# Performance work log

Measured on AMD Instinct MI355X. Metric: run time of the kernel, lower is better.

## Reference

```python
import jax, jax.numpy as jnp
import numpy as np

B, GX, GY = 4, 480, 360
C_IN, C_OUT = 64, 32
N = 480000

def setup_inputs() -> dict:
    key = jax.random.key(0)
    k1, k2, k3, k4, k5 = jax.random.split(key, 5)
    pt_fea = jax.random.normal(k1, (N, C_IN), dtype=jnp.float32)
    pt_ind = jax.random.randint(k2, (N, 2), 0, 360, dtype=jnp.int32)
    batch_idx = jax.random.randint(k3, (N,), 0, B, dtype=jnp.int32)
    W_comp = jax.random.normal(k4, (C_IN, C_OUT), dtype=jnp.float32) * 0.1
    b_comp = jax.random.normal(k5, (C_OUT,), dtype=jnp.float32) * 0.1
    return {"pt_fea": pt_fea, "pt_ind": pt_ind, "batch_idx": batch_idx,
            "W_comp": W_comp, "b_comp": b_comp}

def reference(pt_fea, pt_ind, batch_idx, W_comp, b_comp):
    # Linearized voxel key: (batch, x, y) -> flat segment id.
    # torch.unique + scatter_max over unique voxels followed by fancy-index
    # scatter into a zero grid is equivalent to a dense segment_max with
    # empty voxels forced to zero.
    seg = (batch_idx.astype(jnp.int32) * (GX * GY)
           + pt_ind[:, 0] * GY + pt_ind[:, 1])  # [N]
    num_seg = B * GX * GY
    pooled = jax.ops.segment_max(pt_fea, seg, num_segments=num_seg)  # [BV, C_IN]
    cnt = jax.ops.segment_sum(jnp.ones((pt_fea.shape[0],), jnp.float32), seg,
                              num_segments=num_seg)  # [BV]
    occupied = (cnt > 0)[:, None]
    pooled = jnp.where(occupied, pooled, 0.0)  # neutralize -inf of empty voxels
    # fea_compression: Linear + ReLU, applied to occupied voxels only
    comp = jax.nn.relu(pooled @ W_comp + b_comp)  # [BV, C_OUT]
    comp = jnp.where(occupied, comp, 0.0)
    out = comp.reshape(B, GX, GY, C_OUT)
    return jnp.transpose(out, (0, 3, 1, 2))  # [B, C_OUT, GX, GY]
```

## Files before the change

### kernel.cpp

```cpp
#include <hip/hip_runtime.h>

#define GXGY  172800
#define NSEG  691200
#define CIN   64
#define COUT  32
#define VPB   64
#define PSTR  65
#define NTILE 675


__global__ __launch_bounds__(256) void count_kernel(
    const int* __restrict__ ind,
    const int* __restrict__ bidx,
    int*       __restrict__ cnt,
    int N)
{
    int i = blockIdx.x * 256 + threadIdx.x;
    if (i >= N) return;
    int2 xy = ((const int2*)ind)[i];
    int seg = bidx[i] * GXGY + xy.x * 360 + xy.y;
    atomicAdd(&cnt[seg], 1);
}

__global__ __launch_bounds__(256) void scan_tile_kernel(
    int* __restrict__ cnt, int* __restrict__ tsum)
{
    int t = threadIdx.x;
    int base = blockIdx.x * 256 + t;
    int4 c = ((const int4*)cnt)[base];
    int s = c.x + c.y + c.z + c.w;

    int lane = t & 63, wid = t >> 6;
    int v = s;
    #pragma unroll
    for (int d = 1; d < 64; d <<= 1) {
        int u = __shfl_up(v, d);
        if (lane >= d) v += u;
    }
    __shared__ int wsum[4];
    if (lane == 63) wsum[wid] = v;
    __syncthreads();
    int wbase = 0;
    #pragma unroll
    for (int w = 0; w < 3; ++w) if (w < wid) wbase += wsum[w];

    int excl = wbase + v - s;
    int4 o; o.x = excl; o.y = o.x + c.x; o.z = o.y + c.y; o.w = o.z + c.z;
    ((int4*)cnt)[base] = o;
    if (t == 255) tsum[blockIdx.x] = excl + s;
}

__global__ __launch_bounds__(256) void scan_totals_kernel(int* __restrict__ tsum)
{
    __shared__ int buf[1024];
    int t = threadIdx.x;
    for (int j = t; j < 1024; j += 256) buf[j] = (j < NTILE) ? tsum[j] : 0;
    __syncthreads();
    for (int d = 1; d < 1024; d <<= 1) {
        int vals[4];
        #pragma unroll
        for (int k = 0; k < 4; ++k) { int j = t + k * 256; vals[k] = (j >= d) ? buf[j - d] : 0; }
        __syncthreads();
        #pragma unroll
        for (int k = 0; k < 4; ++k) { int j = t + k * 256; buf[j] += vals[k]; }
        __syncthreads();
    }
    for (int j = t; j < NTILE; j += 256) tsum[j] = (j == 0) ? 0 : buf[j - 1];
}

__global__ __launch_bounds__(256) void fill_kernel(
    const int* __restrict__ ind,
    const int* __restrict__ bidx,
    int*       __restrict__ cnt,
    const int* __restrict__ tsum,
    int*       __restrict__ csr,
    int N)
{
    int i = blockIdx.x * 256 + threadIdx.x;
    if (i >= N) return;
    int2 xy = ((const int2*)ind)[i];
    int seg = bidx[i] * GXGY + xy.x * 360 + xy.y;
    int pos = atomicAdd(&cnt[seg], 1) + tsum[seg >> 10];
    csr[pos] = i;
}

__global__ __launch_bounds__(256) void pool_compress_kernel(
    const float* __restrict__ fea,
    const int*   __restrict__ cnt,
    const int*   __restrict__ tsum,
    const int*   __restrict__ csr,
    const float* __restrict__ W,
    const float* __restrict__ bias,
    float*       __restrict__ out)
{
    __shared__ float sP[VPB * PSTR];
    __shared__ int   sLen[VPB];
    __shared__ int   sIdx[4][64];

    int tid  = threadIdx.x;
    int wid  = tid >> 6;
    int lane = tid & 63;
    int sub  = lane >> 4;
    int sl   = lane & 15;

    int vbase = blockIdx.x * VPB;
    int v0    = vbase + wid * 16;

    int o = 0;
    if (lane < 17) {
        int vv = v0 - 1 + lane;
        o = (vv < 0) ? 0 : (cnt[vv] + tsum[vv >> 10]);
    }
    int onext = __shfl(o, (lane + 1) & 63);
    if (lane < 16) sLen[wid * 16 + lane] = onext - o;

    int ws0 = __shfl(o, 0);
    int wsE = __shfl(o, 16);
    int cw  = wsE - ws0;
    if (lane < min(cw, 64)) sIdx[wid][lane] = csr[ws0 + lane];

    int stt[4], len[4];
    #pragma unroll
    for (int q = 0; q < 4; ++q) {
        int a = __shfl(o, q * 4 + sub);
        int b = __shfl(o, q * 4 + sub + 1);
        stt[q] = a; len[q] = b - a;
    }
    int maxlen = max(max(len[0], len[1]), max(len[2], len[3]));

    float4 m[4];
    #pragma unroll
    for (int q = 0; q < 4; ++q) if (len[q] > 0) {
        int off = stt[q] - ws0;
        int id  = (off < 64) ? sIdx[wid][off] : csr[stt[q]];
        m[q] = ((const float4*)(fea + (size_t)id * CIN))[sl];
    }
    for (int r = 1; r < maxlen; ++r) {
        #pragma unroll
        for (int q = 0; q < 4; ++q) if (r < len[q]) {
            int off = stt[q] - ws0 + r;
            int id  = (off < 64) ? sIdx[wid][off] : csr[stt[q] + r];
            float4 t = ((const float4*)(fea + (size_t)id * CIN))[sl];
            m[q].x = fmaxf(m[q].x, t.x);
            m[q].y = fmaxf(m[q].y, t.y);
            m[q].z = fmaxf(m[q].z, t.z);
            m[q].w = fmaxf(m[q].w, t.w);
        }
    }
    #pragma unroll
    for (int q = 0; q < 4; ++q) if (len[q] > 0) {
        int lv = wid * 16 + q * 4 + sub;
        float* dst = &sP[lv * PSTR + sl * 4];
        dst[0] = m[q].x; dst[1] = m[q].y; dst[2] = m[q].z; dst[3] = m[q].w;
    }
    __syncthreads();

    int lv = lane;
    int g  = __builtin_amdgcn_readfirstlane(wid);
    int b  = vbase / GXGY;
    int rem = vbase - b * GXGY + lv;

    const float* Wg = W + g * 8;
    const float* bg = bias + g * 8;

    float res[8];
    if (sLen[lv] > 0) {
        float acc[8];
        #pragma unroll
        for (int c = 0; c < 8; ++c) acc[c] = bg[c];
        #pragma unroll 16
        for (int k = 0; k < CIN; ++k) {
            float p = sP[lv * PSTR + k];
            #pragma unroll
            for (int c = 0; c < 8; ++c)
                acc[c] = fmaf(p, Wg[k * COUT + c], acc[c]);
        }
        #pragma unroll
        for (int c = 0; c < 8; ++c) res[c] = fmaxf(acc[c], 0.0f);
    } else {
        #pragma unroll
        for (int c = 0; c < 8; ++c) res[c] = 0.0f;
    }

    float* op = out + (size_t)b * COUT * GXGY + (size_t)g * 8 * GXGY + rem;
    #pragma unroll
    for (int c = 0; c < 8; ++c) op[c * GXGY] = res[c];
}

extern "C" void kernel_launch(void* const* d_in, const int* in_sizes, int n_in,
                              void* d_out, int out_size, void* d_ws, size_t ws_size,
                              hipStream_t stream)
{
    const float* fea  = (const float*)d_in[0];
    const int*   ind  = (const int*)d_in[1];
    const int*   bidx = (const int*)d_in[2];
    const float* W    = (const float*)d_in[3];
    const float* bias = (const float*)d_in[4];
    float*       out  = (float*)d_out;

    int N = in_sizes[0] / CIN;

    int* cnt  = (int*)d_ws;
    int* tsum = cnt + NSEG;
    int* csr  = tsum + 1024;

    hipMemsetAsync(cnt, 0, (size_t)NSEG * sizeof(int), stream);
    count_kernel<<<(N + 255) / 256, 256, 0, stream>>>(ind, bidx, cnt, N);
    scan_tile_kernel<<<NTILE, 256, 0, stream>>>(cnt, tsum);
    scan_totals_kernel<<<1, 256, 0, stream>>>(tsum);
    fill_kernel<<<(N + 255) / 256, 256, 0, stream>>>(ind, bidx, cnt, tsum, csr, N);
    pool_compress_kernel<<<NSEG / VPB, 256, 0, stream>>>(fea, cnt, tsum, csr, W, bias, out);
}
```

Before: 294.8 us.

## Fold tile offsets into counts and batch gather loads for more memory-level parallelism

Adds a kernel that adds per-tile scan bases into the count array, so the fill and pool kernels no longer read tsum on every access. The pool kernel's gather loop for the common case (all of a wave's point indices cached in LDS) now issues 16 independent feature loads per iteration using clamped, branch-free indexing, which raises the number of memory requests in flight. Clamped lanes reload rows they already hold, adding redundant loads, and the change costs one extra kernel launch.

```diff
diff --git a/kernel.cpp b/kernel.cpp
--- a/kernel.cpp
+++ b/kernel.cpp
@@ -68,11 +68,20 @@
     for (int j = t; j < NTILE; j += 256) tsum[j] = (j == 0) ? 0 : buf[j - 1];
 }
 
+__global__ __launch_bounds__(256) void add_base_kernel(
+    int* __restrict__ cnt, const int* __restrict__ tsum)
+{
+    int t = tsum[blockIdx.x];
+    int4* p = (int4*)cnt + blockIdx.x * 256 + threadIdx.x;
+    int4 v = *p;
+    v.x += t; v.y += t; v.z += t; v.w += t;
+    *p = v;
+}
+
 __global__ __launch_bounds__(256) void fill_kernel(
     const int* __restrict__ ind,
     const int* __restrict__ bidx,
     int*       __restrict__ cnt,
-    const int* __restrict__ tsum,
     int*       __restrict__ csr,
     int N)
 {
@@ -80,14 +89,13 @@
     if (i >= N) return;
     int2 xy = ((const int2*)ind)[i];
     int seg = bidx[i] * GXGY + xy.x * 360 + xy.y;
-    int pos = atomicAdd(&cnt[seg], 1) + tsum[seg >> 10];
+    int pos = atomicAdd(&cnt[seg], 1);
     csr[pos] = i;
 }
 
 __global__ __launch_bounds__(256) void pool_compress_kernel(
     const float* __restrict__ fea,
     const int*   __restrict__ cnt,
-    const int*   __restrict__ tsum,
     const int*   __restrict__ csr,
     const float* __restrict__ W,
     const float* __restrict__ bias,
@@ -109,7 +117,7 @@
     int o = 0;
     if (lane < 17) {
         int vv = v0 - 1 + lane;
-        o = (vv < 0) ? 0 : (cnt[vv] + tsum[vv >> 10]);
+        o = (vv < 0) ? 0 : cnt[vv];
     }
     int onext = __shfl(o, (lane + 1) & 63);
     if (lane < 16) sLen[wid * 16 + lane] = onext - o;
@@ -122,29 +130,65 @@
     int stt[4], len[4];
     #pragma unroll
     for (int q = 0; q < 4; ++q) {
-        int a = __shfl(o, q * 4 + sub);
-        int b = __shfl(o, q * 4 + sub + 1);
-        stt[q] = a; len[q] = b - a;
+        int a  = __shfl(o, q * 4 + sub);
+        int bb = __shfl(o, q * 4 + sub + 1);
+        stt[q] = a; len[q] = bb - a;
     }
     int maxlen = max(max(len[0], len[1]), max(len[2], len[3]));
 
     float4 m[4];
-    #pragma unroll
-    for (int q = 0; q < 4; ++q) if (len[q] > 0) {
-        int off = stt[q] - ws0;
-        int id  = (off < 64) ? sIdx[wid][off] : csr[stt[q]];
-        m[q] = ((const float4*)(fea + (size_t)id * CIN))[sl];
-    }
-    for (int r = 1; r < maxlen; ++r) {
-        #pragma unroll
-        for (int q = 0; q < 4; ++q) if (r < len[q]) {
-            int off = stt[q] - ws0 + r;
-            int id  = (off < 64) ? sIdx[wid][off] : csr[stt[q] + r];
-            float4 t = ((const float4*)(fea + (size_t)id * CIN))[sl];
-            m[q].x = fmaxf(m[q].x, t.x);
-            m[q].y = fmaxf(m[q].y, t.y);
-            m[q].z = fmaxf(m[q].z, t.z);
-            m[q].w = fmaxf(m[q].w, t.w);
+    if (cw > 0 && cw <= 64) {
+        int s_[4], e_[4];
+        #pragma unroll
+        for (int q = 0; q < 4; ++q) {
+            int b0 = stt[q] - ws0;
+            s_[q] = min(b0, cw - 1);
+            int last = b0 + ((len[q] > 0) ? (len[q] - 1) : 0);
+            e_[q] = min(last, cw - 1);
+        }
+        #pragma unroll
+        for (int q = 0; q < 4; ++q) {
+            int id = sIdx[wid][s_[q]];
+            m[q] = ((const float4*)(fea + (size_t)id * CIN))[sl];
+        }
+        for (int r = 1; r < maxlen; r += 4) {
+            float4 t[4][4];
+            #pragma unroll
+            for (int k = 0; k < 4; ++k) {
+                #pragma unroll
+                for (int q = 0; q < 4; ++q) {
+                    int off = min(s_[q] + r + k, e_[q]);
+                    int id  = sIdx[wid][off];
+                    t[k][q] = ((const float4*)(fea + (size_t)id * CIN))[sl];
+                }
+            }
+            #pragma unroll
+            for (int k = 0; k < 4; ++k) {
+                #pragma unroll
+                for (int q = 0; q < 4; ++q) {
+                    m[q].x = fmaxf(m[q].x, t[k][q].x);
+                    m[q].y = fmaxf(m[q].y, t[k][q].y);
+                    m[q].z = fmaxf(m[q].z, t[k][q].z);
+                    m[q].w = fmaxf(m[q].w, t[k][q].w);
+                }
+            }
+        }
+    } else if (cw > 64) {
+        #pragma unroll
+        for (int q = 0; q < 4; ++q) if (len[q] > 0) {
+            int id = csr[stt[q]];
+            m[q] = ((const float4*)(fea + (size_t)id * CIN))[sl];
+        }
+        for (int r = 1; r < maxlen; ++r) {
+            #pragma unroll
+            for (int q = 0; q < 4; ++q) if (r < len[q]) {
+                int id = csr[stt[q] + r];
+                float4 t = ((const float4*)(fea + (size_t)id * CIN))[sl];
+                m[q].x = fmaxf(m[q].x, t.x);
+                m[q].y = fmaxf(m[q].y, t.y);
+                m[q].z = fmaxf(m[q].z, t.z);
+                m[q].w = fmaxf(m[q].w, t.w);
+            }
         }
     }
     #pragma unroll
@@ -208,6 +252,7 @@
     count_kernel<<<(N + 255) / 256, 256, 0, stream>>>(ind, bidx, cnt, N);
     scan_tile_kernel<<<NTILE, 256, 0, stream>>>(cnt, tsum);
     scan_totals_kernel<<<1, 256, 0, stream>>>(tsum);
-    fill_kernel<<<(N + 255) / 256, 256, 0, stream>>>(ind, bidx, cnt, tsum, csr, N);
-    pool_compress_kernel<<<NSEG / VPB, 256, 0, stream>>>(fea, cnt, tsum, csr, W, bias, out);
-}
+    add_base_kernel<<<NTILE, 256, 0, stream>>>(cnt, tsum);
+    fill_kernel<<<(N + 255) / 256, 256, 0, stream>>>(ind, bidx, cnt, csr, N);
+    pool_compress_kernel<<<NSEG / VPB, 256, 0, stream>>>(fea, cnt, csr, W, bias, out);
+}
```

New measurement: 292.1 us. No clear change (-0.9%).
